# Kernel tuning notes

Hardware: AMD Instinct MI355X
Metric: run time of the kernel (lower is better)

Reference implementation:

```python
import jax, jax.numpy as jnp
import numpy as np

BOS = 1  # tokenizer.bos_token_id


def lstm_cell(x, h, c, Wih, Whh, b):
    # torch LSTM gate order: i, f, g, o
    g = x @ Wih.T + h @ Whh.T + b
    i, f, gg, o = jnp.split(g, 4, axis=-1)
    c2 = jax.nn.sigmoid(f) * c + jax.nn.sigmoid(i) * jnp.tanh(gg)
    h2 = jax.nn.sigmoid(o) * jnp.tanh(c2)
    return h2, c2


def run_lstm_layer(xs, h0, c0, Wih, Whh, b):
    # xs: [T, B, D] -> hs: [T, B, H], final (h, c)
    def step(carry, x):
        h, c = lstm_cell(x, carry[0], carry[1], Wih, Whh, b)
        return (h, c), h
    (h, c), hs = jax.lax.scan(step, (h0, c0), xs)
    return hs, h, c


def setup_inputs() -> dict:
    key = jax.random.key(0)
    ks = jax.random.split(key, 17)
    B, T, E, H, V = 32, 128, 512, 1024, 32000
    s = 0.03  # ~ torch LSTM uniform(-1/sqrt(H), 1/sqrt(H)) scale
    def p(k, shape):
        return jax.random.normal(k, shape, jnp.float32) * s
    return {
        "src": jax.random.randint(ks[0], (B, T), 0, V),
        "emb": p(ks[1], (V, E)),
        "enc_Wih0": p(ks[2], (4 * H, E)),
        "enc_Whh0": p(ks[3], (4 * H, H)),
        "enc_b0": p(ks[4], (4 * H,)),
        "enc_Wih1": p(ks[5], (4 * H, H)),
        "enc_Whh1": p(ks[6], (4 * H, H)),
        "enc_b1": p(ks[7], (4 * H,)),
        "dec_Wih0": p(ks[8], (4 * H, E)),
        "dec_Whh0": p(ks[9], (4 * H, H)),
        "dec_b0": p(ks[10], (4 * H,)),
        "dec_Wih1": p(ks[11], (4 * H, H)),
        "dec_Whh1": p(ks[12], (4 * H, H)),
        "dec_b1": p(ks[13], (4 * H,)),
        "out_W": p(ks[14], (V, H)),
        "out_b": p(ks[15], (V,)),
        "max_len": 64,
    }


def reference(src, emb, enc_Wih0, enc_Whh0, enc_b0, enc_Wih1, enc_Whh1, enc_b1,
              dec_Wih0, dec_Whh0, dec_b0, dec_Wih1, dec_Whh1, dec_b1,
              out_W, out_b, max_len):
    B = src.shape[0]
    H = enc_Whh0.shape[1]
    z = jnp.zeros((B, H), emb.dtype)
    # --- encoder: 2-layer LSTM over src ---
    xs = emb[src].transpose(1, 0, 2)            # [T, B, E]
    hs0, eh0, ec0 = run_lstm_layer(xs, z, z, enc_Wih0, enc_Whh0, enc_b0)
    _, eh1, ec1 = run_lstm_layer(hs0, z, z, enc_Wih1, enc_Whh1, enc_b1)
    tok0 = jnp.full((B,), BOS, jnp.int32)
    def dec_step(carry, _):
        h0, c0, h1, c1, tok = carry
        x = emb[tok]                             # [B, E]
        h0, c0 = lstm_cell(x, h0, c0, dec_Wih0, dec_Whh0, dec_b0)
        h1, c1 = lstm_cell(h0, h1, c1, dec_Wih1, dec_Whh1, dec_b1)
        logits = h1 @ out_W.T + out_b            # [B, V]
        tok = jnp.argmax(logits, axis=-1).astype(jnp.int32)
        return (h0, c0, h1, c1, tok), logits
    _, logits = jax.lax.scan(dec_step, (eh0, ec0, eh1, ec1, tok0), None, length=max_len)
    return logits.transpose(1, 0, 2)             # [B, max_len, V]
```

## Files before the change

kernel.cpp:

```cpp
#include <hip/hip_runtime.h>

typedef unsigned int u32;

constexpr int Bc = 32;
constexpr int Tc = 128;
constexpr int Ec = 512;
constexpr int Hc = 1024;
constexpr int Vc = 32000;
constexpr int Lc = 64;

__device__ __forceinline__ void ldf8(const float* p, float* x) {
    float4 a = *(const float4*)p;
    float4 b = *(const float4*)(p + 4);
    x[0] = a.x; x[1] = a.y; x[2] = a.z; x[3] = a.w;
    x[4] = b.x; x[5] = b.y; x[6] = b.z; x[7] = b.w;
}
__device__ __forceinline__ float sigm(float x) { return 1.0f / (1.0f + expf(-x)); }

__global__ void init_k(float* st, int n, int* tok) {
    int i = blockIdx.x * blockDim.x + threadIdx.x;
    for (; i < n; i += gridDim.x * blockDim.x) st[i] = 0.0f;
    if (blockIdx.x == 0 && threadIdx.x < Bc) tok[threadIdx.x] = 1;
}

template<int KX, int XMODE>
__global__ __launch_bounds__(256)
void cell_k(const float* __restrict__ Wih, const float* __restrict__ Whh,
            const float* __restrict__ bias,
            const float* __restrict__ xbuf, const float* __restrict__ emb,
            const int* __restrict__ src, int tcol, const int* __restrict__ tok,
            const float* __restrict__ h_in, float* __restrict__ h_out,
            float* __restrict__ c)
{
    const int tid = threadIdx.x;
    const int q   = tid >> 6;
    const int oid = tid & 63;
    const int b   = oid & 31;
    const int hj  = oid >> 5;
    const int hk  = blockIdx.x * 2 + hj;

    const float* w0 = Wih + (size_t)(0 * Hc + hk) * KX;
    const float* w1 = Wih + (size_t)(1 * Hc + hk) * KX;
    const float* w2 = Wih + (size_t)(2 * Hc + hk) * KX;
    const float* w3 = Wih + (size_t)(3 * Hc + hk) * KX;
    const float* u0 = Whh + (size_t)(0 * Hc + hk) * Hc;
    const float* u1 = Whh + (size_t)(1 * Hc + hk) * Hc;
    const float* u2 = Whh + (size_t)(2 * Hc + hk) * Hc;
    const float* u3 = Whh + (size_t)(3 * Hc + hk) * Hc;

    float a0 = 0.f, a1 = 0.f, a2 = 0.f, a3 = 0.f;
    float xv[8], w[8];

    const float* xrow = nullptr;
    if constexpr (XMODE == 0) {
        xrow = xbuf + b * KX;
    } else if constexpr (XMODE == 1) {
        xrow = emb + (size_t)src[b * Tc + tcol] * Ec;
    } else {
        xrow = emb + (size_t)tok[b] * Ec;
    }
    {
        const int kq = KX / 4;
        for (int k = q * kq; k < q * kq + kq; k += 8) {
            ldf8(xrow + k, xv);
            ldf8(w0 + k, w);
            #pragma unroll
            for (int i = 0; i < 8; i++) a0 += w[i] * xv[i];
            ldf8(w1 + k, w);
            #pragma unroll
            for (int i = 0; i < 8; i++) a1 += w[i] * xv[i];
            ldf8(w2 + k, w);
            #pragma unroll
            for (int i = 0; i < 8; i++) a2 += w[i] * xv[i];
            ldf8(w3 + k, w);
            #pragma unroll
            for (int i = 0; i < 8; i++) a3 += w[i] * xv[i];
        }
    }
    {
        const float* hrow = h_in + b * Hc;
        const int kq = Hc / 4;
        for (int k = q * kq; k < q * kq + kq; k += 8) {
            ldf8(hrow + k, xv);
            ldf8(u0 + k, w);
            #pragma unroll
            for (int i = 0; i < 8; i++) a0 += w[i] * xv[i];
            ldf8(u1 + k, w);
            #pragma unroll
            for (int i = 0; i < 8; i++) a1 += w[i] * xv[i];
            ldf8(u2 + k, w);
            #pragma unroll
            for (int i = 0; i < 8; i++) a2 += w[i] * xv[i];
            ldf8(u3 + k, w);
            #pragma unroll
            for (int i = 0; i < 8; i++) a3 += w[i] * xv[i];
        }
    }

    __shared__ float red[4][64][4];
    red[q][oid][0] = a0; red[q][oid][1] = a1;
    red[q][oid][2] = a2; red[q][oid][3] = a3;
    __syncthreads();
    if (q == 0) {
        #pragma unroll
        for (int qq = 1; qq < 4; qq++) {
            a0 += red[qq][oid][0]; a1 += red[qq][oid][1];
            a2 += red[qq][oid][2]; a3 += red[qq][oid][3];
        }
        a0 += bias[0 * Hc + hk];
        a1 += bias[1 * Hc + hk];
        a2 += bias[2 * Hc + hk];
        a3 += bias[3 * Hc + hk];
        const float ig = sigm(a0), fg = sigm(a1);
        const float gv = tanhf(a2), og = sigm(a3);
        const int idx = b * Hc + hk;
        const float cn = fg * c[idx] + ig * gv;
        c[idx] = cn;
        h_out[idx] = og * tanhf(cn);
    }
}

__global__ __launch_bounds__(256)
void logits_k(const float* __restrict__ h1, const float* __restrict__ outW,
              const float* __restrict__ outb, float* __restrict__ out, int s,
              float* __restrict__ pmax, int* __restrict__ pidx)
{
    __shared__ float hl[32][68];
    __shared__ float sval[256];
    __shared__ int   sidx[256];
    const int tid = threadIdx.x;
    const int bq  = tid >> 3;
    const int vl  = tid & 7;
    const int v0  = blockIdx.x * 64;

    float acc[8];
    #pragma unroll
    for (int j = 0; j < 8; j++) acc[j] = 0.f;

    const float* wbase = outW + (size_t)(v0 + vl * 8) * Hc;

    for (int kc = 0; kc < 16; kc++) {
        #pragma unroll
        for (int i = 0; i < 2; i++) {
            const int idx4 = tid + i * 256;
            const int bb = idx4 >> 4, kq = idx4 & 15;
            *(float4*)&hl[bb][kq * 4] =
                *(const float4*)(h1 + bb * Hc + kc * 64 + kq * 4);
        }
        __syncthreads();
        #pragma unroll
        for (int i8 = 0; i8 < 8; i8++) {
            float h8[8];
            *(float4*)&h8[0] = *(const float4*)&hl[bq][i8 * 8];
            *(float4*)&h8[4] = *(const float4*)&hl[bq][i8 * 8 + 4];
            const float* wk = wbase + kc * 64 + i8 * 8;
            #pragma unroll
            for (int j = 0; j < 8; j++) {
                float w[8]; ldf8(wk + (size_t)j * Hc, w);
                float t = acc[j];
                #pragma unroll
                for (int i = 0; i < 8; i++) t += w[i] * h8[i];
                acc[j] = t;
            }
        }
        __syncthreads();
    }

    float best = -3.4e38f; int bidx = 0;
    alignas(16) float ob[8];
    #pragma unroll
    for (int j = 0; j < 8; j++) {
        const int v = v0 + vl * 8 + j;
        const float val = acc[j] + outb[v];
        ob[j] = val;
        if (val > best) { best = val; bidx = v; }
    }
    float* dst = out + (size_t)(bq * Lc + s) * Vc + v0 + vl * 8;
    *(float4*)dst       = *(const float4*)&ob[0];
    *(float4*)(dst + 4) = *(const float4*)&ob[4];

    sval[tid] = best; sidx[tid] = bidx;
    __syncthreads();
    if (vl == 0) {
        #pragma unroll
        for (int u = 1; u < 8; u++) {
            const float v2 = sval[tid + u]; const int i2 = sidx[tid + u];
            if (v2 > best || (v2 == best && i2 < bidx)) { best = v2; bidx = i2; }
        }
        pmax[blockIdx.x * 32 + bq] = best;
        pidx[blockIdx.x * 32 + bq] = bidx;
    }
}

__global__ __launch_bounds__(256)
void argmax_fin_k(const float* __restrict__ pmax, const int* __restrict__ pidx,
                  int* __restrict__ tok)
{
    __shared__ float sv[256];
    __shared__ int   si[256];
    const int b = blockIdx.x, tid = threadIdx.x;
    float best = -3.4e38f; int bidx = 0x7fffffff;
    for (int j = tid; j < 500; j += 256) {
        const float v = pmax[j * 32 + b]; const int i = pidx[j * 32 + b];
        if (v > best || (v == best && i < bidx)) { best = v; bidx = i; }
    }
    sv[tid] = best; si[tid] = bidx;
    __syncthreads();
    for (int st = 128; st > 0; st >>= 1) {
        if (tid < st) {
            const float v = sv[tid + st]; const int i = si[tid + st];
            if (v > sv[tid] || (v == sv[tid] && i < si[tid])) { sv[tid] = v; si[tid] = i; }
        }
        __syncthreads();
    }
    if (tid == 0) tok[b] = si[0];
}

extern "C" void kernel_launch(void* const* d_in, const int* in_sizes, int n_in,
                              void* d_out, int out_size, void* d_ws, size_t ws_size,
                              hipStream_t stream)
{
    const int*   src = (const int*)d_in[0];
    const float* emb = (const float*)d_in[1];
    const float* eW0 = (const float*)d_in[2];
    const float* eU0 = (const float*)d_in[3];
    const float* eb0 = (const float*)d_in[4];
    const float* eW1 = (const float*)d_in[5];
    const float* eU1 = (const float*)d_in[6];
    const float* eb1 = (const float*)d_in[7];
    const float* dW0 = (const float*)d_in[8];
    const float* dU0 = (const float*)d_in[9];
    const float* db0 = (const float*)d_in[10];
    const float* dW1 = (const float*)d_in[11];
    const float* dU1 = (const float*)d_in[12];
    const float* db1 = (const float*)d_in[13];
    const float* oW  = (const float*)d_in[14];
    const float* obv = (const float*)d_in[15];
    float* out = (float*)d_out;

    float* ws   = (float*)d_ws;
    float* h0   = ws;
    float* c0   = ws + 65536;
    float* h1   = ws + 98304;
    float* c1   = ws + 163840;
    int*   tok  = (int*)(ws + 196608);
    float* pmax = ws + 196672;
    int*   pidx = (int*)(ws + 212672);

    init_k<<<128, 256, 0, stream>>>(ws, 196608, tok);

    for (int t = 0; t < Tc; t++) {
        const int r = t & 1, w = 1 - r;
        cell_k<Ec, 1><<<512, 256, 0, stream>>>(
            eW0, eU0, eb0, nullptr, emb, src, t, nullptr,
            h0 + r * 32768, h0 + w * 32768, c0);
        cell_k<Hc, 0><<<512, 256, 0, stream>>>(
            eW1, eU1, eb1, h0 + w * 32768, nullptr, nullptr, 0, nullptr,
            h1 + r * 32768, h1 + w * 32768, c1);
    }

    for (int s = 0; s < Lc; s++) {
        const int r = s & 1, w = 1 - r;
        cell_k<Ec, 2><<<512, 256, 0, stream>>>(
            dW0, dU0, db0, nullptr, emb, nullptr, 0, tok,
            h0 + r * 32768, h0 + w * 32768, c0);
        cell_k<Hc, 0><<<512, 256, 0, stream>>>(
            dW1, dU1, db1, h0 + w * 32768, nullptr, nullptr, 0, nullptr,
            h1 + r * 32768, h1 + w * 32768, c1);
        logits_k<<<500, 256, 0, stream>>>(
            h1 + w * 32768, oW, obv, out, s, pmax, pidx);
        argmax_fin_k<<<32, 256, 0, stream>>>(pmax, pidx, tok);
    }
    (void)in_sizes; (void)n_in; (void)out_size; (void)ws_size;
}
```

Before: 51.04 ms.

## Fuse all LSTM steps into one persistent kernel with grid-wide barriers

Replaces roughly 640 separate kernel launches (encoder cells, decoder cells, logits, argmax) with a single persistent kernel of 512 blocks. The phases are separated by a software grid barrier built on atomic counter and generation variables. This removes per-launch overhead and gaps between the many small sequential kernels. In exchange it depends on all 512 blocks being co-resident (launch bounds 256,2 on 256 CUs), or the barrier deadlocks. Each barrier also costs atomic traffic and spinning.

```diff
diff --git a/kernel.cpp b/kernel.cpp
--- a/kernel.cpp
+++ b/kernel.cpp
@@ -8,6 +8,7 @@
 constexpr int Hc = 1024;
 constexpr int Vc = 32000;
 constexpr int Lc = 64;
+constexpr int NBLK = 512;
 
 __device__ __forceinline__ void ldf8(const float* p, float* x) {
     float4 a = *(const float4*)p;
@@ -17,20 +18,41 @@
 }
 __device__ __forceinline__ float sigm(float x) { return 1.0f / (1.0f + expf(-x)); }
 
-__global__ void init_k(float* st, int n, int* tok) {
-    int i = blockIdx.x * blockDim.x + threadIdx.x;
-    for (; i < n; i += gridDim.x * blockDim.x) st[i] = 0.0f;
-    if (blockIdx.x == 0 && threadIdx.x < Bc) tok[threadIdx.x] = 1;
+__device__ __align__(128) u32 g_cnt = 0;
+__device__ __align__(128) u32 g_gen = 0;
+
+__device__ __forceinline__ void gsync() {
+    __syncthreads();
+    if (threadIdx.x == 0) {
+        __threadfence();
+        const u32 g = __hip_atomic_load(&g_gen, __ATOMIC_RELAXED,
+                                        __HIP_MEMORY_SCOPE_AGENT);
+        const u32 old = __hip_atomic_fetch_add(&g_cnt, 1u, __ATOMIC_ACQ_REL,
+                                               __HIP_MEMORY_SCOPE_AGENT);
+        if (old == NBLK - 1) {
+            __hip_atomic_store(&g_cnt, 0u, __ATOMIC_RELAXED,
+                               __HIP_MEMORY_SCOPE_AGENT);
+            __hip_atomic_fetch_add(&g_gen, 1u, __ATOMIC_RELEASE,
+                                   __HIP_MEMORY_SCOPE_AGENT);
+        } else {
+            while (__hip_atomic_load(&g_gen, __ATOMIC_RELAXED,
+                                     __HIP_MEMORY_SCOPE_AGENT) == g) {
+                __builtin_amdgcn_s_sleep(2);
+            }
+        }
+        __threadfence();
+    }
+    __syncthreads();
 }
 
 template<int KX, int XMODE>
-__global__ __launch_bounds__(256)
-void cell_k(const float* __restrict__ Wih, const float* __restrict__ Whh,
-            const float* __restrict__ bias,
-            const float* __restrict__ xbuf, const float* __restrict__ emb,
-            const int* __restrict__ src, int tcol, const int* __restrict__ tok,
-            const float* __restrict__ h_in, float* __restrict__ h_out,
-            float* __restrict__ c)
+__device__ __forceinline__ void cell_phase(
+    const float* __restrict__ Wih, const float* __restrict__ Whh,
+    const float* __restrict__ bias,
+    const float* __restrict__ xbuf, const float* __restrict__ emb,
+    const int* __restrict__ src, int tcol, const int* __restrict__ tok,
+    const float* __restrict__ h_in, float* __restrict__ h_out,
+    float* __restrict__ c, float (&red)[4][64][4])
 {
     const int tid = threadIdx.x;
     const int q   = tid >> 6;
@@ -97,7 +119,6 @@
         }
     }
 
-    __shared__ float red[4][64][4];
     red[q][oid][0] = a0; red[q][oid][1] = a1;
     red[q][oid][2] = a2; red[q][oid][3] = a3;
     __syncthreads();
@@ -120,14 +141,12 @@
     }
 }
 
-__global__ __launch_bounds__(256)
-void logits_k(const float* __restrict__ h1, const float* __restrict__ outW,
-              const float* __restrict__ outb, float* __restrict__ out, int s,
-              float* __restrict__ pmax, int* __restrict__ pidx)
-{
-    __shared__ float hl[32][68];
-    __shared__ float sval[256];
-    __shared__ int   sidx[256];
+__device__ __forceinline__ void logits_phase(
+    const float* __restrict__ h1, const float* __restrict__ outW,
+    const float* __restrict__ outb, float* __restrict__ out, int s,
+    float* __restrict__ pmax, int* __restrict__ pidx,
+    float (&hl)[32][68], float (&sval)[256], int (&sidx)[256])
+{
     const int tid = threadIdx.x;
     const int bq  = tid >> 3;
     const int vl  = tid & 7;
@@ -192,12 +211,10 @@
     }
 }
 
-__global__ __launch_bounds__(256)
-void argmax_fin_k(const float* __restrict__ pmax, const int* __restrict__ pidx,
-                  int* __restrict__ tok)
-{
-    __shared__ float sv[256];
-    __shared__ int   si[256];
+__device__ __forceinline__ void argmax_phase(
+    const float* __restrict__ pmax, const int* __restrict__ pidx,
+    int* __restrict__ tok, float (&sv)[256], int (&si)[256])
+{
     const int b = blockIdx.x, tid = threadIdx.x;
     float best = -3.4e38f; int bidx = 0x7fffffff;
     for (int j = tid; j < 500; j += 256) {
@@ -214,6 +231,65 @@
         __syncthreads();
     }
     if (tid == 0) tok[b] = si[0];
+}
+
+__global__ __launch_bounds__(256, 2)
+void seq2seq_k(const int* __restrict__ src, const float* __restrict__ emb,
+               const float* __restrict__ eW0, const float* __restrict__ eU0,
+               const float* __restrict__ eb0, const float* __restrict__ eW1,
+               const float* __restrict__ eU1, const float* __restrict__ eb1,
+               const float* __restrict__ dW0, const float* __restrict__ dU0,
+               const float* __restrict__ db0, const float* __restrict__ dW1,
+               const float* __restrict__ dU1, const float* __restrict__ db1,
+               const float* __restrict__ oW,  const float* __restrict__ obv,
+               float* __restrict__ out, float* __restrict__ ws)
+{
+    float* h0   = ws;
+    float* c0   = ws + 65536;
+    float* h1   = ws + 98304;
+    float* c1   = ws + 163840;
+    int*   tok  = (int*)(ws + 196608);
+    float* pmax = ws + 196672;
+    int*   pidx = (int*)(ws + 212672);
+
+    __shared__ float red[4][64][4];
+    __shared__ float hl[32][68];
+    __shared__ float sval[256];
+    __shared__ int   sidx[256];
+
+    {
+        int i = blockIdx.x * blockDim.x + threadIdx.x;
+        for (; i < 196608; i += gridDim.x * blockDim.x) ws[i] = 0.0f;
+        if (blockIdx.x == 0 && threadIdx.x < Bc) tok[threadIdx.x] = 1;
+    }
+    gsync();
+
+    for (int t = 0; t < Tc; t++) {
+        const int r = t & 1, w = 1 - r;
+        cell_phase<Ec, 1>(eW0, eU0, eb0, nullptr, emb, src, t, nullptr,
+                          h0 + r * 32768, h0 + w * 32768, c0, red);
+        gsync();
+        cell_phase<Hc, 0>(eW1, eU1, eb1, h0 + w * 32768, nullptr, nullptr, 0,
+                          nullptr, h1 + r * 32768, h1 + w * 32768, c1, red);
+        gsync();
+    }
+
+    for (int s = 0; s < Lc; s++) {
+        const int r = s & 1, w = 1 - r;
+        cell_phase<Ec, 2>(dW0, dU0, db0, nullptr, emb, nullptr, 0, tok,
+                          h0 + r * 32768, h0 + w * 32768, c0, red);
+        gsync();
+        cell_phase<Hc, 0>(dW1, dU1, db1, h0 + w * 32768, nullptr, nullptr, 0,
+                          nullptr, h1 + r * 32768, h1 + w * 32768, c1, red);
+        gsync();
+        if (blockIdx.x < 500)
+            logits_phase(h1 + w * 32768, oW, obv, out, s, pmax, pidx,
+                         hl, sval, sidx);
+        gsync();
+        if (blockIdx.x < Bc)
+            argmax_phase(pmax, pidx, tok, sval, sidx);
+        gsync();
+    }
 }
 
 extern "C" void kernel_launch(void* const* d_in, const int* in_sizes, int n_in,
@@ -237,39 +313,11 @@
     const float* oW  = (const float*)d_in[14];
     const float* obv = (const float*)d_in[15];
     float* out = (float*)d_out;
-
-    float* ws   = (float*)d_ws;
-    float* h0   = ws;
-    float* c0   = ws + 65536;
-    float* h1   = ws + 98304;
-    float* c1   = ws + 163840;
-    int*   tok  = (int*)(ws + 196608);
-    float* pmax = ws + 196672;
-    int*   pidx = (int*)(ws + 212672);
-
-    init_k<<<128, 256, 0, stream>>>(ws, 196608, tok);
-
-    for (int t = 0; t < Tc; t++) {
-        const int r = t & 1, w = 1 - r;
-        cell_k<Ec, 1><<<512, 256, 0, stream>>>(
-            eW0, eU0, eb0, nullptr, emb, src, t, nullptr,
-            h0 + r * 32768, h0 + w * 32768, c0);
-        cell_k<Hc, 0><<<512, 256, 0, stream>>>(
-            eW1, eU1, eb1, h0 + w * 32768, nullptr, nullptr, 0, nullptr,
-            h1 + r * 32768, h1 + w * 32768, c1);
-    }
-
-    for (int s = 0; s < Lc; s++) {
-        const int r = s & 1, w = 1 - r;
-        cell_k<Ec, 2><<<512, 256, 0, stream>>>(
-            dW0, dU0, db0, nullptr, emb, nullptr, 0, tok,
-            h0 + r * 32768, h0 + w * 32768, c0);
-        cell_k<Hc, 0><<<512, 256, 0, stream>>>(
-            dW1, dU1, db1, h0 + w * 32768, nullptr, nullptr, 0, nullptr,
-            h1 + r * 32768, h1 + w * 32768, c1);
-        logits_k<<<500, 256, 0, stream>>>(
-            h1 + w * 32768, oW, obv, out, s, pmax, pidx);
-        argmax_fin_k<<<32, 256, 0, stream>>>(pmax, pidx, tok);
-    }
+    float* ws  = (float*)d_ws;
+
+    seq2seq_k<<<dim3(NBLK), dim3(256), 0, stream>>>(
+        src, emb, eW0, eU0, eb0, eW1, eU1, eb1,
+        dW0, dU0, db0, dW1, dU1, db1, oW, obv, out, ws);
+
     (void)in_sizes; (void)n_in; (void)out_size; (void)ws_size;
 }
```

New measurement: 68.33 ms. 33.9% more time.
